# Performance work log

Measured on AMD Instinct MI355X. Metric: run time of the kernel, lower is better.

The kernel has to match this reference:

```python
import jax, jax.numpy as jnp
import numpy as np

BATCH, NODE, DIM = 4, 2048, 128
EPS = 1e-5


def _bn(x, gamma, beta):
    # BatchNorm1d in training mode: biased batch stats over rows, per-feature.
    mu = jnp.mean(x, axis=0)
    var = jnp.var(x, axis=0)
    return (x - mu) * jax.lax.rsqrt(var + EPS) * gamma + beta


def setup_inputs() -> dict:
    key = jax.random.key(0)
    ks = jax.random.split(key, 8)
    N = BATCH * NODE
    # Scale L like a normalized graph operator so activations stay sane.
    L = jax.random.normal(ks[0], (N, N), dtype=jnp.float32) / np.sqrt(N)
    inputs = jax.random.normal(ks[1], (BATCH, NODE, DIM), dtype=jnp.float32)
    mask = jnp.zeros((BATCH, NODE, 1), dtype=bool)  # unused in forward
    lim = 1.0 / np.sqrt(2 * DIM)
    fc0_w = jax.random.uniform(ks[2], (DIM, 2 * DIM), jnp.float32, -lim, lim)
    fc0_b = jax.random.uniform(ks[3], (DIM,), jnp.float32, -lim, lim)
    fc1_w = jax.random.uniform(ks[4], (DIM, 2 * DIM), jnp.float32, -lim, lim)
    fc1_b = jax.random.uniform(ks[5], (DIM,), jnp.float32, -lim, lim)
    bn0_gamma = jnp.ones((2 * DIM,), jnp.float32)
    bn0_beta = jnp.zeros((2 * DIM,), jnp.float32)
    bn1_gamma = jnp.ones((2 * DIM,), jnp.float32)
    bn1_beta = jnp.zeros((2 * DIM,), jnp.float32)
    return dict(L=L, mask=mask, inputs=inputs,
                bn0_gamma=bn0_gamma, bn0_beta=bn0_beta, fc0_w=fc0_w, fc0_b=fc0_b,
                bn1_gamma=bn1_gamma, bn1_beta=bn1_beta, fc1_w=fc1_w, fc1_b=fc1_b)


def reference(L, mask, inputs, bn0_gamma, bn0_beta, fc0_w, fc0_b,
              bn1_gamma, bn1_beta, fc1_w, fc1_b):
    b, n, d = inputs.shape

    def block(x, gamma, beta, w, bias):
        # x: (b, n, d). Laplacian propagation over flattened batch*node dim.
        xf = x.reshape(-1, d)                      # (b*n, d)
        Lx = (L @ xf).reshape(b, n, d)
        h = jnp.concatenate([x, Lx], axis=2).reshape(-1, 2 * d)
        h = _bn(h, gamma, beta)                    # pre-BN
        h = h @ w.T + bias                         # Linear(2d -> d)
        return h.reshape(b, n, d)

    x = jax.nn.elu(inputs)
    x = block(x, bn0_gamma, bn0_beta, fc0_w, fc0_b)
    x = jax.nn.elu(x)
    x = block(x, bn1_gamma, bn1_beta, fc1_w, fc1_b)
    return x + inputs
```

## Files before the change

### kernel.cpp

```cpp
#include <hip/hip_runtime.h>
#include <math.h>

#define NROWS 8192
#define DIM   128
#define FEAT  256
#define BK    128
#define NT    (NROWS / BK)

typedef __attribute__((ext_vector_type(8))) __bf16 bf16x8;
typedef __attribute__((ext_vector_type(8))) unsigned short u16x8;
typedef __attribute__((ext_vector_type(4))) unsigned short u16x4;
typedef __attribute__((ext_vector_type(4))) float f32x4;

__device__ __forceinline__ float bf2f(unsigned short h) {
  return __uint_as_float(((unsigned)h) << 16);
}
__device__ __forceinline__ unsigned short f2bf(float f) {
  unsigned u = __float_as_uint(f);
  return (unsigned short)((u + 0x7fff + ((u >> 16) & 1)) >> 16);
}
__device__ __forceinline__ void async16(const void* g, void* l) {
  __builtin_amdgcn_global_load_lds(
      (const __attribute__((address_space(1))) void*)g,
      (__attribute__((address_space(3))) void*)l, 16, 0, 0);
}
__device__ __forceinline__ f32x4 mfma16(bf16x8 a, bf16x8 b, f32x4 c) {
  return __builtin_amdgcn_mfma_f32_16x16x32_bf16(a, b, c, 0, 0, 0);
}
__device__ __forceinline__ float ldp(const void* p, int i, int is32) {
  return is32 ? ((const float*)p)[i] : bf2f(((const unsigned short*)p)[i]);
}

__global__ void detect_kernel(const unsigned short* __restrict__ L,
                              int* __restrict__ flag,
                              float* __restrict__ stats)
{
  for (int i = threadIdx.x; i < 1024; i += 256) stats[i] = 0.f;
  __shared__ int cnt;
  if (threadIdx.x == 0) cnt = 0;
  __syncthreads();
  int c = 0;
  for (int i = 0; i < 16; i++) {
    unsigned short s = L[2 * (threadIdx.x + 256 * i)];
    int e = (s >> 7) & 0xFF;
    if (e >= 192) c++;
  }
  atomicAdd(&cnt, c);
  __syncthreads();
  if (threadIdx.x == 0) *flag = (cnt > 16) ? 1 : 0;
}

__global__ __launch_bounds__(256) void trans_kernel(
    const void* __restrict__ src, unsigned short* __restrict__ xT,
    unsigned short* __restrict__ x0, unsigned short* __restrict__ inpc,
    float* __restrict__ stats, const int* __restrict__ flag,
    const void* __restrict__ w0raw, const void* __restrict__ w1raw,
    unsigned short* __restrict__ wb)
{
  __shared__ __align__(16) unsigned short T[128 * 136];
  const int tid = threadIdx.x;
  const int r0 = blockIdx.x * 128;
  const int is32 = *flag;

  if (blockIdx.x < 8) {
    const int base = blockIdx.x * 8192;
    for (int i = tid; i < 8192; i += 256) {
      const int g = base + i;
      const float v = (g < 32768) ? ldp(w0raw, g, is32)
                                  : ldp(w1raw, g - 32768, is32);
      wb[g] = f2bf(v);
    }
  }

  #pragma unroll
  for (int i = 0; i < 8; i++) {
    const int c = tid + 256 * i;
    const int rr = c >> 4, cg = c & 15;
    const size_t gidx = (size_t)(r0 + rr) * DIM + cg * 8;
    u16x8 v;
    if (is32) {
      const float* s = (const float*)src + gidx;
      f32x4 a = *(const f32x4*)s, b = *(const f32x4*)(s + 4);
      #pragma unroll
      for (int e = 0; e < 4; e++) { v[e] = f2bf(a[e]); v[e + 4] = f2bf(b[e]); }
    } else {
      v = *(const u16x8*)((const unsigned short*)src + gidx);
    }
    *(u16x8*)(inpc + gidx) = v;
    #pragma unroll
    for (int e = 0; e < 8; e++) {
      float f = bf2f(v[e]);
      f = f > 0.f ? f : expm1f(f);
      v[e] = f2bf(f);
    }
    *(u16x8*)(x0 + gidx) = v;
    *(u16x8*)(T + rr * 136 + cg * 8) = v;
  }
  __syncthreads();
  #pragma unroll
  for (int i = 0; i < 8; i++) {
    const int c = tid + 256 * i;
    const int n = c >> 4, mg = c & 15;
    u16x8 v;
    float s = 0.f, q = 0.f;
    #pragma unroll
    for (int e = 0; e < 8; e++) {
      unsigned short h = T[(mg * 8 + e) * 136 + n];
      v[e] = h;
      float f = bf2f(h);
      s += f; q += f * f;
    }
    *(u16x8*)(xT + (size_t)n * NROWS + r0 + mg * 8) = v;
    #pragma unroll
    for (int off = 1; off < 16; off <<= 1) {
      s += __shfl_xor(s, off, 16);
      q += __shfl_xor(q, off, 16);
    }
    if ((tid & 15) == 0) {
      atomicAdd(&stats[n], s);
      atomicAdd(&stats[256 + n], q);
    }
  }
}

template <int IS32>
__device__ __forceinline__ void gemm1_body(
    const void* __restrict__ Lraw, const unsigned short* __restrict__ xT,
    unsigned short* __restrict__ Lxb, float* __restrict__ stats,
    unsigned short* __restrict__ AsBase, unsigned short* __restrict__ BsBase)
{
  const int tid  = threadIdx.x;
  const int lane = tid & 63;
  const int wave = tid >> 6;
  const int wm = wave >> 2, wn = wave & 3;
  const int ln = lane & 15, quad = lane >> 4;
  const int m0 = blockIdx.x * 32;

  const int arow = tid >> 4, ap = tid & 15;
  const int akg = (ap & 8) | ((ap & 7) ^ (arow & 7));
  const float*          Lf = (const float*)Lraw;
  const unsigned short* Lh = (const unsigned short*)Lraw;
  const size_t Abase = (size_t)(m0 + arow) * NROWS + akg * 8;

  int brow[4], bkg[4];
  #pragma unroll
  for (int i = 0; i < 4; i++) {
    const int c = tid + (i << 9);
    brow[i] = c >> 4;
    const int p = c & 15;
    bkg[i] = (p & 8) | ((p & 7) ^ (brow[i] & 7));
  }

  unsigned short* a0 = AsBase;
  unsigned short* a1 = AsBase + 32 * 128;
  unsigned short* a2 = AsBase + 2 * 32 * 128;
  unsigned short* c0 = BsBase;
  unsigned short* c1 = BsBase + 128 * 128;
  unsigned short* c2 = BsBase + 2 * 128 * 128;

  f32x4 acc[2];
  acc[0] = (f32x4){0.f, 0.f, 0.f, 0.f};
  acc[1] = (f32x4){0.f, 0.f, 0.f, 0.f};

  auto issueB = [&](int kt, unsigned short* Bbuf) {
    const size_t koff = (size_t)kt * BK;
    #pragma unroll
    for (int i = 0; i < 4; i++) {
      const int c = tid + (i << 9);
      async16(xT + (size_t)brow[i] * NROWS + koff + bkg[i] * 8, Bbuf + c * 8);
    }
  };
  auto loadA = [&](int kt, f32x4& r0, f32x4& r1) {
    const float* s = Lf + Abase + (size_t)kt * BK;
    r0 = *(const f32x4*)s;
    r1 = *(const f32x4*)(s + 4);
  };
  auto issueA16 = [&](int kt, unsigned short* Abuf) {
    async16(Lh + Abase + (size_t)kt * BK, Abuf + arow * 128 + ap * 8);
  };
  auto writeA = [&](const f32x4& r0, const f32x4& r1, unsigned short* Abuf) {
    u16x8 o;
    #pragma unroll
    for (int e = 0; e < 4; e++) { o[e] = f2bf(r0[e]); o[e + 4] = f2bf(r1[e]); }
    *(u16x8*)(Abuf + arow * 128 + ap * 8) = o;
  };
  auto compute = [&](const unsigned short* Abuf, const unsigned short* Bbuf) {
    const int arf = wm * 16 + ln;
    const int brf = wn * 32 + ln;
    __builtin_amdgcn_s_setprio(1);
    #pragma unroll
    for (int ks = 0; ks < 4; ks++) {
      const int kga = ks * 4 + quad;
      bf16x8 af = *(const bf16x8*)(Abuf + arf * 128 +
                     ((kga & 8) | ((kga & 7) ^ (arf & 7))) * 8);
      #pragma unroll
      for (int j = 0; j < 2; j++) {
        const int rb = brf + j * 16;
        bf16x8 bf = *(const bf16x8*)(Bbuf + rb * 128 +
                       ((kga & 8) | ((kga & 7) ^ (rb & 7))) * 8);
        acc[j] = mfma16(af, bf, acc[j]);
      }
    }
    __builtin_amdgcn_s_setprio(0);
  };
  auto waitbar = [&]() {
    if (IS32) asm volatile("s_waitcnt vmcnt(6) lgkmcnt(0)" ::: "memory");
    else      asm volatile("s_waitcnt vmcnt(5) lgkmcnt(0)" ::: "memory");
    __builtin_amdgcn_s_barrier();
  };

  f32x4 e0, e1, o0, o1;

  issueB(0, c0);
  if (IS32) loadA(0, e0, e1); else issueA16(0, a0);
  issueB(1, c1);
  if (IS32) loadA(1, o0, o1); else issueA16(1, a1);
  if (IS32) writeA(e0, e1, a0);
  waitbar();

  for (int p = 0; p < 31; ++p) {
    const int t = 2 * p;
    issueB(t + 2, c2);
    if (IS32) loadA(t + 2, e0, e1); else issueA16(t + 2, a2);
    compute(a0, c0);
    if (IS32) writeA(o0, o1, a1);
    waitbar();
    issueB(t + 3, c0);
    if (IS32) loadA(t + 3, o0, o1); else issueA16(t + 3, a0);
    compute(a1, c1);
    if (IS32) writeA(e0, e1, a2);
    waitbar();
    unsigned short* tB = c2; c2 = c1; c1 = c0; c0 = tB;
    unsigned short* tA = a2; a2 = a1; a1 = a0; a0 = tA;
  }

  compute(a0, c0);
  if (IS32) writeA(o0, o1, a1);
  __syncthreads();
  compute(a1, c1);
  __syncthreads();

  float* E = (float*)AsBase;
  #pragma unroll
  for (int j = 0; j < 2; j++) {
    const int col = wn * 32 + j * 16 + ln;
    #pragma unroll
    for (int r = 0; r < 4; r++)
      E[(wm * 16 + quad * 4 + r) * 128 + col] = acc[j][r];
  }
  __syncthreads();
  {
    const int row = tid >> 4, cc0 = (tid & 15) * 8;
    u16x8 o;
    #pragma unroll
    for (int e = 0; e < 8; e++) o[e] = f2bf(E[row * 128 + cc0 + e]);
    *(u16x8*)(Lxb + (size_t)(m0 + row) * DIM + cc0) = o;
  }
  if (tid < 128) {
    float s = 0.f, q = 0.f;
    #pragma unroll
    for (int r = 0; r < 32; r++) {
      const float v = E[r * 128 + tid];
      s += v; q += v * v;
    }
    atomicAdd(&stats[128 + tid], s);
    atomicAdd(&stats[384 + tid], q);
  }
}

__global__ __launch_bounds__(512) void gemm1_fused(
    const void* __restrict__ Lraw, const unsigned short* __restrict__ xT,
    unsigned short* __restrict__ Lxb, float* __restrict__ stats,
    const int* __restrict__ flag)
{
  __shared__ __align__(16) unsigned short As[3 * 32 * 128];
  __shared__ __align__(16) unsigned short Bs[3 * 128 * 128];
  if (*flag) gemm1_body<1>(Lraw, xT, Lxb, stats, As, Bs);
  else       gemm1_body<0>(Lraw, xT, Lxb, stats, As, Bs);
}

__global__ __launch_bounds__(256) void gemm2_fc(
    const unsigned short* __restrict__ xb,
    const unsigned short* __restrict__ Lxb,
    const unsigned short* __restrict__ wb,
    const void* __restrict__ gamma, const void* __restrict__ beta,
    const void* __restrict__ bias,
    const float* __restrict__ stats,
    const unsigned short* __restrict__ resid,
    void* __restrict__ outv,
    unsigned short* __restrict__ xTout,
    float* __restrict__ statsOut,
    int mode, const int* __restrict__ flag)
{
  __shared__ __align__(16) unsigned short As[32 * 264];
  __shared__ float sS[256], sMS[256], bred[256], bv[128];
  const int is32 = *flag;
  const int tid = threadIdx.x;
  const int lane = tid & 63, wave = tid >> 6;
  const int m0 = blockIdx.x * 32;

  {
    const int j = tid;
    const float inv = 1.f / 8192.f;
    const float mu = stats[j] * inv;
    const float var = fmaxf(stats[256 + j] * inv - mu * mu, 0.f);
    const float sj = ldp(gamma, j, is32) * rsqrtf(var + 1e-5f);
    sS[j] = sj;
    sMS[j] = mu * sj;
  }
  {
    const int k = tid & 127, half = tid >> 7;
    float a = 0.f;
    #pragma unroll
    for (int jj = 0; jj < 128; jj += 8) {
      u16x8 wv = *(const u16x8*)(wb + k * 256 + half * 128 + jj);
      #pragma unroll
      for (int e = 0; e < 8; e++)
        a += ldp(beta, half * 128 + jj + e, is32) * bf2f(wv[e]);
    }
    bred[tid] = a;
  }
  __syncthreads();
  if (tid < 128)
    bv[tid] = ldp(bias, tid, is32) + bred[tid] + bred[tid + 128];

  #pragma unroll
  for (int i = 0; i < 4; i++) {
    const int c = tid + 256 * i;
    const int mr = c >> 5, ch = c & 31;
    const unsigned short* src =
        (ch < 16) ? (xb  + (size_t)(m0 + mr) * DIM + ch * 8)
                  : (Lxb + (size_t)(m0 + mr) * DIM + (ch - 16) * 8);
    u16x8 v = *(const u16x8*)src;
    const int j0 = ch * 8;
    #pragma unroll
    for (int e = 0; e < 8; e++) {
      const float f = bf2f(v[e]);
      v[e] = f2bf(f * sS[j0 + e] - sMS[j0 + e]);
    }
    *(u16x8*)(As + mr * 264 + ch * 8) = v;
  }
  __syncthreads();

  const int ln = lane & 15, quad = lane >> 4;
  const int nq = wave * 32;
  f32x4 acc[2][2];
  #pragma unroll
  for (int i = 0; i < 2; i++)
    #pragma unroll
    for (int j = 0; j < 2; j++)
      acc[i][j] = (f32x4){0.f, 0.f, 0.f, 0.f};

  #pragma unroll
  for (int ks = 0; ks < 8; ks++) {
    bf16x8 af[2], bfr[2];
    #pragma unroll
    for (int i = 0; i < 2; i++)
      af[i] = *(const bf16x8*)(As + (i * 16 + ln) * 264 + ks * 32 + quad * 8);
    #pragma unroll
    for (int j = 0; j < 2; j++)
      bfr[j] = *(const bf16x8*)(wb + (size_t)(nq + j * 16 + ln) * FEAT +
                                ks * 32 + quad * 8);
    #pragma unroll
    for (int i = 0; i < 2; i++)
      #pragma unroll
      for (int j = 0; j < 2; j++)
        acc[i][j] = mfma16(af[i], bfr[j], acc[i][j]);
  }

  #pragma unroll
  for (int j = 0; j < 2; j++) {
    const int gn = nq + j * 16 + ln;
    const float bb = bv[gn];
    float s = 0.f, q = 0.f;
    #pragma unroll
    for (int i = 0; i < 2; i++) {
      u16x4 pk;
      #pragma unroll
      for (int r = 0; r < 4; r++) {
        const int gm = m0 + i * 16 + quad * 4 + r;
        float v = acc[i][j][r] + bb;
        const size_t idx = (size_t)gm * DIM + gn;
        if (mode == 0) {
          v = v > 0.f ? v : expm1f(v);
          const unsigned short h = f2bf(v);
          ((unsigned short*)outv)[idx] = h;
          pk[r] = h;
          const float hv = bf2f(h);
          s += hv; q += hv * hv;
        } else {
          v += bf2f(resid[idx]);
          if (is32) ((float*)outv)[idx] = v;
          else      ((unsigned short*)outv)[idx] = f2bf(v);
        }
      }
      if (mode == 0)
        *(u16x4*)(xTout + (size_t)gn * NROWS + m0 + i * 16 + quad * 4) = pk;
    }
    if (mode == 0) {
      s += __shfl_xor(s, 16); q += __shfl_xor(q, 16);
      s += __shfl_xor(s, 32); q += __shfl_xor(q, 32);
      if (quad == 0) {
        atomicAdd(&statsOut[gn], s);
        atomicAdd(&statsOut[256 + gn], q);
      }
    }
  }
}

extern "C" void kernel_launch(void* const* d_in, const int* in_sizes, int n_in,
                              void* d_out, int out_size, void* d_ws, size_t ws_size,
                              hipStream_t stream) {
  const void* Lm   = d_in[0];
  const void* inp  = d_in[2];
  const void* bn0g = d_in[3];
  const void* bn0b = d_in[4];
  const void* fc0w = d_in[5];
  const void* fc0b = d_in[6];
  const void* bn1g = d_in[7];
  const void* bn1b = d_in[8];
  const void* fc1w = d_in[9];
  const void* fc1b = d_in[10];

  char* ws = (char*)d_ws;
  unsigned short* xT   = (unsigned short*)(ws);
  unsigned short* x0   = (unsigned short*)(ws + (2ull << 20));
  unsigned short* Lxb  = (unsigned short*)(ws + (4ull << 20));
  unsigned short* x1   = (unsigned short*)(ws + (6ull << 20));
  unsigned short* inpc = (unsigned short*)(ws + (8ull << 20));
  float*          stats= (float*)         (ws + (10ull << 20));
  int*            flag = (int*)           (ws + (10ull << 20) + 8192);
  unsigned short* wb   = (unsigned short*)(ws + (10ull << 20) + 16384);

  detect_kernel<<<1, 256, 0, stream>>>((const unsigned short*)Lm, flag, stats);

  trans_kernel<<<64, 256, 0, stream>>>(inp, xT, x0, inpc, stats, flag,
                                       fc0w, fc1w, wb);
  gemm1_fused<<<256, 512, 0, stream>>>(Lm, xT, Lxb, stats, flag);
  gemm2_fc<<<256, 256, 0, stream>>>(x0, Lxb, wb, bn0g, bn0b, fc0b,
                                    stats, nullptr, x1,
                                    xT, stats + 512, 0, flag);

  gemm1_fused<<<256, 512, 0, stream>>>(Lm, xT, Lxb, stats + 512, flag);
  gemm2_fc<<<256, 256, 0, stream>>>(x1, Lxb, wb + 32768, bn1g, bn1b, fc1b,
                                    stats + 512, inpc, d_out,
                                    nullptr, nullptr, 1, flag);
}
```

Measured before the change: 207.2 us.

## Fuse all stages into one cooperative persistent kernel with grid syncs

Replaces the six separate launches (detect, transpose, two L-GEMMs, two FC GEMMs) with a single cooperative kernel of 256 blocks x 512 threads that separates the phases with grid.sync. The transpose and FC phases are re-split to 32 rows per block and 8 waves to match the new shape. Every block now runs the dtype detection itself, and the setprio hints are removed from the GEMM inner loop. The aim is to remove launch gaps between stages. In exchange, grid-wide barriers are added, all phases share one 512-thread shape with a large shared-memory footprint, and the cooperative launch depends on all 256 blocks fitting on the device at once.

```diff
diff --git a/kernel.cpp b/kernel.cpp
--- a/kernel.cpp
+++ b/kernel.cpp
@@ -1,5 +1,8 @@
 #include <hip/hip_runtime.h>
+#include <hip/hip_cooperative_groups.h>
 #include <math.h>
+
+namespace cg = cooperative_groups;
 
 #define NROWS 8192
 #define DIM   128
@@ -31,51 +34,15 @@
   return is32 ? ((const float*)p)[i] : bf2f(((const unsigned short*)p)[i]);
 }
 
-__global__ void detect_kernel(const unsigned short* __restrict__ L,
-                              int* __restrict__ flag,
-                              float* __restrict__ stats)
-{
-  for (int i = threadIdx.x; i < 1024; i += 256) stats[i] = 0.f;
-  __shared__ int cnt;
-  if (threadIdx.x == 0) cnt = 0;
-  __syncthreads();
-  int c = 0;
-  for (int i = 0; i < 16; i++) {
-    unsigned short s = L[2 * (threadIdx.x + 256 * i)];
-    int e = (s >> 7) & 0xFF;
-    if (e >= 192) c++;
-  }
-  atomicAdd(&cnt, c);
-  __syncthreads();
-  if (threadIdx.x == 0) *flag = (cnt > 16) ? 1 : 0;
-}
-
-__global__ __launch_bounds__(256) void trans_kernel(
+__device__ __forceinline__ void trans_phase(
     const void* __restrict__ src, unsigned short* __restrict__ xT,
     unsigned short* __restrict__ x0, unsigned short* __restrict__ inpc,
-    float* __restrict__ stats, const int* __restrict__ flag,
-    const void* __restrict__ w0raw, const void* __restrict__ w1raw,
-    unsigned short* __restrict__ wb)
+    float* __restrict__ stats, int is32, char* smemraw, int bid, int tid)
 {
-  __shared__ __align__(16) unsigned short T[128 * 136];
-  const int tid = threadIdx.x;
-  const int r0 = blockIdx.x * 128;
-  const int is32 = *flag;
-
-  if (blockIdx.x < 8) {
-    const int base = blockIdx.x * 8192;
-    for (int i = tid; i < 8192; i += 256) {
-      const int g = base + i;
-      const float v = (g < 32768) ? ldp(w0raw, g, is32)
-                                  : ldp(w1raw, g - 32768, is32);
-      wb[g] = f2bf(v);
-    }
-  }
-
-  #pragma unroll
-  for (int i = 0; i < 8; i++) {
-    const int c = tid + 256 * i;
-    const int rr = c >> 4, cg = c & 15;
+  unsigned short* T = (unsigned short*)smemraw;
+  const int r0 = bid * 32;
+  {
+    const int rr = tid >> 4, cg = tid & 15;
     const size_t gidx = (size_t)(r0 + rr) * DIM + cg * 8;
     u16x8 v;
     if (is32) {
@@ -97,10 +64,8 @@
     *(u16x8*)(T + rr * 136 + cg * 8) = v;
   }
   __syncthreads();
-  #pragma unroll
-  for (int i = 0; i < 8; i++) {
-    const int c = tid + 256 * i;
-    const int n = c >> 4, mg = c & 15;
+  {
+    const int n = tid >> 2, mg = tid & 3;
     u16x8 v;
     float s = 0.f, q = 0.f;
     #pragma unroll
@@ -112,11 +77,11 @@
     }
     *(u16x8*)(xT + (size_t)n * NROWS + r0 + mg * 8) = v;
     #pragma unroll
-    for (int off = 1; off < 16; off <<= 1) {
-      s += __shfl_xor(s, off, 16);
-      q += __shfl_xor(q, off, 16);
-    }
-    if ((tid & 15) == 0) {
+    for (int off = 1; off < 4; off <<= 1) {
+      s += __shfl_xor(s, off, 4);
+      q += __shfl_xor(q, off, 4);
+    }
+    if ((tid & 3) == 0) {
       atomicAdd(&stats[n], s);
       atomicAdd(&stats[256 + n], q);
     }
@@ -187,7 +152,6 @@
   auto compute = [&](const unsigned short* Abuf, const unsigned short* Bbuf) {
     const int arf = wm * 16 + ln;
     const int brf = wn * 32 + ln;
-    __builtin_amdgcn_s_setprio(1);
     #pragma unroll
     for (int ks = 0; ks < 4; ks++) {
       const int kga = ks * 4 + quad;
@@ -201,7 +165,6 @@
         acc[j] = mfma16(af, bf, acc[j]);
       }
     }
-    __builtin_amdgcn_s_setprio(0);
   };
   auto waitbar = [&]() {
     if (IS32) asm volatile("s_waitcnt vmcnt(6) lgkmcnt(0)" ::: "memory");
@@ -268,18 +231,7 @@
   }
 }
 
-__global__ __launch_bounds__(512) void gemm1_fused(
-    const void* __restrict__ Lraw, const unsigned short* __restrict__ xT,
-    unsigned short* __restrict__ Lxb, float* __restrict__ stats,
-    const int* __restrict__ flag)
-{
-  __shared__ __align__(16) unsigned short As[3 * 32 * 128];
-  __shared__ __align__(16) unsigned short Bs[3 * 128 * 128];
-  if (*flag) gemm1_body<1>(Lraw, xT, Lxb, stats, As, Bs);
-  else       gemm1_body<0>(Lraw, xT, Lxb, stats, As, Bs);
-}
-
-__global__ __launch_bounds__(256) void gemm2_fc(
+__device__ __forceinline__ void gemm2_phase(
     const unsigned short* __restrict__ xb,
     const unsigned short* __restrict__ Lxb,
     const unsigned short* __restrict__ wb,
@@ -290,16 +242,17 @@
     void* __restrict__ outv,
     unsigned short* __restrict__ xTout,
     float* __restrict__ statsOut,
-    int mode, const int* __restrict__ flag)
+    int mode, int is32, char* smemraw, int bid, int tid)
 {
-  __shared__ __align__(16) unsigned short As[32 * 264];
-  __shared__ float sS[256], sMS[256], bred[256], bv[128];
-  const int is32 = *flag;
-  const int tid = threadIdx.x;
+  unsigned short* As = (unsigned short*)smemraw;
+  float* sS   = (float*)(smemraw + 20480);
+  float* sMS  = sS + 256;
+  float* bred = sMS + 256;
+  float* bv   = bred + 512;
   const int lane = tid & 63, wave = tid >> 6;
-  const int m0 = blockIdx.x * 32;
-
-  {
+  const int m0 = bid * 32;
+
+  if (tid < 256) {
     const int j = tid;
     const float inv = 1.f / 8192.f;
     const float mu = stats[j] * inv;
@@ -309,24 +262,25 @@
     sMS[j] = mu * sj;
   }
   {
-    const int k = tid & 127, half = tid >> 7;
+    const int k = tid & 127, qtr = tid >> 7;
     float a = 0.f;
     #pragma unroll
-    for (int jj = 0; jj < 128; jj += 8) {
-      u16x8 wv = *(const u16x8*)(wb + k * 256 + half * 128 + jj);
+    for (int jj = 0; jj < 64; jj += 8) {
+      u16x8 wv = *(const u16x8*)(wb + k * 256 + qtr * 64 + jj);
       #pragma unroll
       for (int e = 0; e < 8; e++)
-        a += ldp(beta, half * 128 + jj + e, is32) * bf2f(wv[e]);
+        a += ldp(beta, qtr * 64 + jj + e, is32) * bf2f(wv[e]);
     }
     bred[tid] = a;
   }
   __syncthreads();
   if (tid < 128)
-    bv[tid] = ldp(bias, tid, is32) + bred[tid] + bred[tid + 128];
+    bv[tid] = ldp(bias, tid, is32) + bred[tid] + bred[tid + 128] +
+              bred[tid + 256] + bred[tid + 384];
 
   #pragma unroll
-  for (int i = 0; i < 4; i++) {
-    const int c = tid + 256 * i;
+  for (int i = 0; i < 2; i++) {
+    const int c = tid + 512 * i;
     const int mr = c >> 5, ch = c & 31;
     const unsigned short* src =
         (ch < 16) ? (xb  + (size_t)(m0 + mr) * DIM + ch * 8)
@@ -343,29 +297,22 @@
   __syncthreads();
 
   const int ln = lane & 15, quad = lane >> 4;
-  const int nq = wave * 32;
-  f32x4 acc[2][2];
-  #pragma unroll
-  for (int i = 0; i < 2; i++)
-    #pragma unroll
-    for (int j = 0; j < 2; j++)
-      acc[i][j] = (f32x4){0.f, 0.f, 0.f, 0.f};
+  const int wm2 = wave >> 2, wn2 = wave & 3;
+  const int nq = wn2 * 32;
+  f32x4 acc[2];
+  acc[0] = (f32x4){0.f, 0.f, 0.f, 0.f};
+  acc[1] = (f32x4){0.f, 0.f, 0.f, 0.f};
 
   #pragma unroll
   for (int ks = 0; ks < 8; ks++) {
-    bf16x8 af[2], bfr[2];
-    #pragma unroll
-    for (int i = 0; i < 2; i++)
-      af[i] = *(const bf16x8*)(As + (i * 16 + ln) * 264 + ks * 32 + quad * 8);
-    #pragma unroll
-    for (int j = 0; j < 2; j++)
-      bfr[j] = *(const bf16x8*)(wb + (size_t)(nq + j * 16 + ln) * FEAT +
-                                ks * 32 + quad * 8);
-    #pragma unroll
-    for (int i = 0; i < 2; i++)
-      #pragma unroll
-      for (int j = 0; j < 2; j++)
-        acc[i][j] = mfma16(af[i], bfr[j], acc[i][j]);
+    bf16x8 af = *(const bf16x8*)(As + (wm2 * 16 + ln) * 264 + ks * 32 +
+                                 quad * 8);
+    #pragma unroll
+    for (int j = 0; j < 2; j++) {
+      bf16x8 bfr = *(const bf16x8*)(wb + (size_t)(nq + j * 16 + ln) * FEAT +
+                                    ks * 32 + quad * 8);
+      acc[j] = mfma16(af, bfr, acc[j]);
+    }
   }
 
   #pragma unroll
@@ -373,31 +320,27 @@
     const int gn = nq + j * 16 + ln;
     const float bb = bv[gn];
     float s = 0.f, q = 0.f;
-    #pragma unroll
-    for (int i = 0; i < 2; i++) {
-      u16x4 pk;
-      #pragma unroll
-      for (int r = 0; r < 4; r++) {
-        const int gm = m0 + i * 16 + quad * 4 + r;
-        float v = acc[i][j][r] + bb;
-        const size_t idx = (size_t)gm * DIM + gn;
-        if (mode == 0) {
-          v = v > 0.f ? v : expm1f(v);
-          const unsigned short h = f2bf(v);
-          ((unsigned short*)outv)[idx] = h;
-          pk[r] = h;
-          const float hv = bf2f(h);
-          s += hv; q += hv * hv;
-        } else {
-          v += bf2f(resid[idx]);
-          if (is32) ((float*)outv)[idx] = v;
-          else      ((unsigned short*)outv)[idx] = f2bf(v);
-        }
+    u16x4 pk;
+    #pragma unroll
+    for (int r = 0; r < 4; r++) {
+      const int gm = m0 + wm2 * 16 + quad * 4 + r;
+      float v = acc[j][r] + bb;
+      const size_t idx = (size_t)gm * DIM + gn;
+      if (mode == 0) {
+        v = v > 0.f ? v : expm1f(v);
+        const unsigned short h = f2bf(v);
+        ((unsigned short*)outv)[idx] = h;
+        pk[r] = h;
+        const float hv = bf2f(h);
+        s += hv; q += hv * hv;
+      } else {
+        v += bf2f(resid[idx]);
+        if (is32) ((float*)outv)[idx] = v;
+        else      ((unsigned short*)outv)[idx] = f2bf(v);
       }
-      if (mode == 0)
-        *(u16x4*)(xTout + (size_t)gn * NROWS + m0 + i * 16 + quad * 4) = pk;
     }
     if (mode == 0) {
+      *(u16x4*)(xTout + (size_t)gn * NROWS + m0 + wm2 * 16 + quad * 4) = pk;
       s += __shfl_xor(s, 16); q += __shfl_xor(q, 16);
       s += __shfl_xor(s, 32); q += __shfl_xor(q, 32);
       if (quad == 0) {
@@ -406,6 +349,77 @@
       }
     }
   }
+}
+
+__global__ __launch_bounds__(512) void fused_all(
+    const void* __restrict__ Lm, const void* __restrict__ inp,
+    const void* __restrict__ bn0g, const void* __restrict__ bn0b,
+    const void* __restrict__ fc0w, const void* __restrict__ fc0b,
+    const void* __restrict__ bn1g, const void* __restrict__ bn1b,
+    const void* __restrict__ fc1w, const void* __restrict__ fc1b,
+    void* __restrict__ d_out,
+    unsigned short* __restrict__ xT, unsigned short* __restrict__ x0,
+    unsigned short* __restrict__ Lxb, unsigned short* __restrict__ x1,
+    unsigned short* __restrict__ inpc,
+    float* __restrict__ stats, unsigned short* __restrict__ wb)
+{
+  __shared__ __align__(16) char smem[122880];
+  __shared__ int cnt;
+  cg::grid_group grid = cg::this_grid();
+  const int tid = threadIdx.x;
+  const int bid = blockIdx.x;
+
+  if (tid == 0) cnt = 0;
+  __syncthreads();
+  {
+    const unsigned short* u = (const unsigned short*)Lm;
+    int c = 0;
+    #pragma unroll
+    for (int i = 0; i < 8; i++) {
+      int e = (u[tid * 8 + i] >> 7) & 0xFF;
+      if (e >= 192) c++;
+    }
+    atomicAdd(&cnt, c);
+  }
+  __syncthreads();
+  const int is32 = (cnt > 16);
+  if (bid == 0) { stats[tid] = 0.f; stats[tid + 512] = 0.f; }
+  if (bid < 8) {
+    const int base = bid * 8192;
+    for (int i = tid; i < 8192; i += 512) {
+      const int g = base + i;
+      const float v = (g < 32768) ? ldp(fc0w, g, is32)
+                                  : ldp(fc1w, g - 32768, is32);
+      wb[g] = f2bf(v);
+    }
+  }
+  grid.sync();
+
+  trans_phase(inp, xT, x0, inpc, stats, is32, smem, bid, tid);
+  grid.sync();
+
+  {
+    unsigned short* As = (unsigned short*)smem;
+    unsigned short* Bs = (unsigned short*)(smem + 24576);
+    if (is32) gemm1_body<1>(Lm, xT, Lxb, stats, As, Bs);
+    else      gemm1_body<0>(Lm, xT, Lxb, stats, As, Bs);
+  }
+  grid.sync();
+
+  gemm2_phase(x0, Lxb, wb, bn0g, bn0b, fc0b, stats, nullptr, x1,
+              xT, stats + 512, 0, is32, smem, bid, tid);
+  grid.sync();
+
+  {
+    unsigned short* As = (unsigned short*)smem;
+    unsigned short* Bs = (unsigned short*)(smem + 24576);
+    if (is32) gemm1_body<1>(Lm, xT, Lxb, stats + 512, As, Bs);
+    else      gemm1_body<0>(Lm, xT, Lxb, stats + 512, As, Bs);
+  }
+  grid.sync();
+
+  gemm2_phase(x1, Lxb, wb + 32768, bn1g, bn1b, fc1b, stats + 512, inpc,
+              d_out, nullptr, nullptr, 1, is32, smem, bid, tid);
 }
 
 extern "C" void kernel_launch(void* const* d_in, const int* in_sizes, int n_in,
@@ -429,20 +443,16 @@
   unsigned short* x1   = (unsigned short*)(ws + (6ull << 20));
   unsigned short* inpc = (unsigned short*)(ws + (8ull << 20));
   float*          stats= (float*)         (ws + (10ull << 20));
-  int*            flag = (int*)           (ws + (10ull << 20) + 8192);
   unsigned short* wb   = (unsigned short*)(ws + (10ull << 20) + 16384);
 
-  detect_kernel<<<1, 256, 0, stream>>>((const unsigned short*)Lm, flag, stats);
-
-  trans_kernel<<<64, 256, 0, stream>>>(inp, xT, x0, inpc, stats, flag,
-                                       fc0w, fc1w, wb);
-  gemm1_fused<<<256, 512, 0, stream>>>(Lm, xT, Lxb, stats, flag);
-  gemm2_fc<<<256, 256, 0, stream>>>(x0, Lxb, wb, bn0g, bn0b, fc0b,
-                                    stats, nullptr, x1,
-                                    xT, stats + 512, 0, flag);
-
-  gemm1_fused<<<256, 512, 0, stream>>>(Lm, xT, Lxb, stats + 512, flag);
-  gemm2_fc<<<256, 256, 0, stream>>>(x1, Lxb, wb + 32768, bn1g, bn1b, fc1b,
-                                    stats + 512, inpc, d_out,
-                                    nullptr, nullptr, 1, flag);
-}
+  void* args[] = {
+    (void*)&Lm, (void*)&inp,
+    (void*)&bn0g, (void*)&bn0b, (void*)&fc0w, (void*)&fc0b,
+    (void*)&bn1g, (void*)&bn1b, (void*)&fc1w, (void*)&fc1b,
+    (void*)&d_out,
+    (void*)&xT, (void*)&x0, (void*)&Lxb, (void*)&x1, (void*)&inpc,
+    (void*)&stats, (void*)&wb
+  };
+  hipLaunchCooperativeKernel((const void*)fused_all, dim3(256), dim3(512),
+                             args, 0, stream);
+}
```

Measured after the change: 329.0 us. 58.7% more time.

## Split K across wave halves in L@x GEMM with 2x2 register tiles

Applied to the files above, without the earlier changes.

The wave layout of the big L@x GEMM changes. Instead of splitting 32x128 output tiles by M across two wave groups, each wave group handles half of the K slice and computes a 2x2 block of 16x16 MFMA tiles. The two partial accumulators are then summed through LDS in the epilogue. This raises fragment reuse, with 4 LDS loads per 4 MFMAs instead of 3 per 2, and the fp32-to-bf16 writeA of A is moved before compute. The cost is one extra reduction pass and barrier through shared memory, more accumulator registers, and the loss of the setprio hints.

```diff
diff --git a/kernel.cpp b/kernel.cpp
--- a/kernel.cpp
+++ b/kernel.cpp
@@ -132,7 +132,7 @@
   const int tid  = threadIdx.x;
   const int lane = tid & 63;
   const int wave = tid >> 6;
-  const int wm = wave >> 2, wn = wave & 3;
+  const int kh = wave >> 2, wq = wave & 3;
   const int ln = lane & 15, quad = lane >> 4;
   const int m0 = blockIdx.x * 32;
 
@@ -158,9 +158,12 @@
   unsigned short* c1 = BsBase + 128 * 128;
   unsigned short* c2 = BsBase + 2 * 128 * 128;
 
-  f32x4 acc[2];
-  acc[0] = (f32x4){0.f, 0.f, 0.f, 0.f};
-  acc[1] = (f32x4){0.f, 0.f, 0.f, 0.f};
+  f32x4 acc[2][2];
+  #pragma unroll
+  for (int i = 0; i < 2; i++)
+    #pragma unroll
+    for (int j = 0; j < 2; j++)
+      acc[i][j] = (f32x4){0.f, 0.f, 0.f, 0.f};
 
   auto issueB = [&](int kt, unsigned short* Bbuf) {
     const size_t koff = (size_t)kt * BK;
@@ -185,23 +188,19 @@
     *(u16x8*)(Abuf + arow * 128 + ap * 8) = o;
   };
   auto compute = [&](const unsigned short* Abuf, const unsigned short* Bbuf) {
-    const int arf = wm * 16 + ln;
-    const int brf = wn * 32 + ln;
-    __builtin_amdgcn_s_setprio(1);
-    #pragma unroll
-    for (int ks = 0; ks < 4; ks++) {
-      const int kga = ks * 4 + quad;
-      bf16x8 af = *(const bf16x8*)(Abuf + arf * 128 +
-                     ((kga & 8) | ((kga & 7) ^ (arf & 7))) * 8);
-      #pragma unroll
-      for (int j = 0; j < 2; j++) {
-        const int rb = brf + j * 16;
-        bf16x8 bf = *(const bf16x8*)(Bbuf + rb * 128 +
-                       ((kga & 8) | ((kga & 7) ^ (rb & 7))) * 8);
-        acc[j] = mfma16(af, bf, acc[j]);
-      }
-    }
-    __builtin_amdgcn_s_setprio(0);
+    #pragma unroll
+    for (int s = 0; s < 2; s++) {
+      const int kga = kh * 8 + s * 4 + quad;
+      const int sw8 = ((kga & 8) | ((kga & 7) ^ (ln & 7))) * 8;
+      bf16x8 af0 = *(const bf16x8*)(Abuf + ln * 128 + sw8);
+      bf16x8 af1 = *(const bf16x8*)(Abuf + (16 + ln) * 128 + sw8);
+      bf16x8 bf0 = *(const bf16x8*)(Bbuf + (wq * 32 + ln) * 128 + sw8);
+      bf16x8 bf1 = *(const bf16x8*)(Bbuf + (wq * 32 + 16 + ln) * 128 + sw8);
+      acc[0][0] = mfma16(af0, bf0, acc[0][0]);
+      acc[0][1] = mfma16(af0, bf1, acc[0][1]);
+      acc[1][0] = mfma16(af1, bf0, acc[1][0]);
+      acc[1][1] = mfma16(af1, bf1, acc[1][1]);
+    }
   };
   auto waitbar = [&]() {
     if (IS32) asm volatile("s_waitcnt vmcnt(6) lgkmcnt(0)" ::: "memory");
@@ -222,31 +221,45 @@
     const int t = 2 * p;
     issueB(t + 2, c2);
     if (IS32) loadA(t + 2, e0, e1); else issueA16(t + 2, a2);
+    if (IS32) writeA(o0, o1, a1);
     compute(a0, c0);
-    if (IS32) writeA(o0, o1, a1);
     waitbar();
     issueB(t + 3, c0);
     if (IS32) loadA(t + 3, o0, o1); else issueA16(t + 3, a0);
+    if (IS32) writeA(e0, e1, a2);
     compute(a1, c1);
-    if (IS32) writeA(e0, e1, a2);
     waitbar();
     unsigned short* tB = c2; c2 = c1; c1 = c0; c0 = tB;
     unsigned short* tA = a2; a2 = a1; a1 = a0; a0 = tA;
   }
 
+  if (IS32) writeA(o0, o1, a1);
   compute(a0, c0);
-  if (IS32) writeA(o0, o1, a1);
   __syncthreads();
   compute(a1, c1);
   __syncthreads();
 
   float* E = (float*)AsBase;
-  #pragma unroll
-  for (int j = 0; j < 2; j++) {
-    const int col = wn * 32 + j * 16 + ln;
-    #pragma unroll
-    for (int r = 0; r < 4; r++)
-      E[(wm * 16 + quad * 4 + r) * 128 + col] = acc[j][r];
+  if (kh == 0) {
+    #pragma unroll
+    for (int i = 0; i < 2; i++)
+      #pragma unroll
+      for (int j = 0; j < 2; j++)
+        #pragma unroll
+        for (int r = 0; r < 4; r++)
+          E[(i * 16 + quad * 4 + r) * 128 + wq * 32 + j * 16 + ln] =
+              acc[i][j][r];
+  }
+  __syncthreads();
+  if (kh == 1) {
+    #pragma unroll
+    for (int i = 0; i < 2; i++)
+      #pragma unroll
+      for (int j = 0; j < 2; j++)
+        #pragma unroll
+        for (int r = 0; r < 4; r++)
+          E[(i * 16 + quad * 4 + r) * 128 + wq * 32 + j * 16 + ln] +=
+              acc[i][j][r];
   }
   __syncthreads();
   {
```

Measured after the change: 203.1 us. -2.0%, faster.
